# Performance work log

Hardware: AMD Instinct MI355X
Metric: run time of the kernel (lower is better)

## Reference

```python
import jax, jax.numpy as jnp
import numpy as np

ALPHA = 1.0
EPS = 1e-12  # tf.nn.l2_normalize epsilon


def setup_inputs() -> dict:
    key = jax.random.key(0)
    k1, k2 = jax.random.split(key)
    B, I, J, D, K = 32, 32, 32, 128, 64
    features = jax.random.normal(k1, (B, I, J, D), dtype=jnp.float32)
    kmeans_centers = jax.random.normal(k2, (B, K, D), dtype=jnp.float32)
    return {"features": features, "kmeans_centers": kmeans_centers}


def reference(features, kmeans_centers):
    # features: (B, I, J, D); kmeans_centers: (B, K, D)
    B = features.shape[0]
    # Squared distance ||f - c||^2 expanded to avoid materializing (B,I,J,K,D)
    f2 = jnp.sum(features * features, axis=-1)[..., None]          # (B,I,J,1)
    c2 = jnp.sum(kmeans_centers * kmeans_centers, axis=-1)[:, None, None, :]  # (B,1,1,K)
    fc = jnp.einsum('bijd,bkd->bijk', features, kmeans_centers)     # (B,I,J,K)
    d2 = f2 - 2.0 * fc + c2                                         # (B,I,J,K)
    sim = jax.nn.softmax(-ALPHA * d2, axis=-1)                      # (B,I,J,K)
    # vlad[b,k,d] = sum_ij sim[b,i,j,k] * (f[b,i,j,d] - c[b,k,d])
    vlad = (jnp.einsum('bijk,bijd->bkd', sim, features)
            - jnp.sum(sim, axis=(1, 2))[..., None] * kmeans_centers)  # (B,K,D)
    flat = vlad.reshape(B, -1)                                      # (B, K*D)
    # K.l2_normalize with axis=None -> normalize over ALL elements (global norm)
    norm = jnp.sqrt(jnp.maximum(jnp.sum(flat * flat), EPS))
    return flat / norm
```

## Files before the change

kernel.cpp:

```cpp
#include <hip/hip_runtime.h>


#define NB    32
#define SPLIT 16

typedef short short8 __attribute__((ext_vector_type(8)));
typedef float f32x4  __attribute__((ext_vector_type(4)));

__device__ __forceinline__ float bf2f(unsigned short u) {
    return __uint_as_float(((unsigned)u) << 16);
}
__device__ __forceinline__ unsigned short f2bf(float f) {
    unsigned u = __float_as_uint(f);
    return (unsigned short)((u + 0x7fffu + ((u >> 16) & 1u)) >> 16);
}
__device__ __forceinline__ int swz3(int x) { return (x ^ (x >> 3)) & 7; }

__global__ __launch_bounds__(256, 2)
void netvlad_main(const float* __restrict__ feat,
                  const float* __restrict__ cent,
                  float* __restrict__ partial,
                  float* __restrict__ ssumG)
{
    __shared__ __align__(16) char smem[58624];
    ushort4*        centHi = (ushort4*)smem;
    ushort4*        centLo = (ushort4*)(smem + 16384);
    unsigned short* FT     = (unsigned short*)(smem + 32768);
    unsigned short* ST     = (unsigned short*)(smem + 49152);
    float*          c2L    = (float*)(smem + 57344);
    float*          ssumW  = (float*)(smem + 57600);

    const int tid = threadIdx.x;
    const int bs  = blockIdx.x;
    const int b   = bs >> 4;
    const int n0  = (bs & 15) * 64;

    const float4* cent4 = (const float4*)cent + (size_t)b * 2048;
    const float4* feat4 = (const float4*)feat + ((size_t)b * 1024 + n0) * 32;

    #pragma unroll
    for (int it = 0; it < 8; ++it) {
        int g  = it * 256 + tid;
        int k  = g >> 5;
        int d4 = g & 31;
        float4 v = cent4[g];
        ushort4 h, l;
        h.x = f2bf(v.x); l.x = f2bf(v.x - bf2f(h.x));
        h.y = f2bf(v.y); l.y = f2bf(v.y - bf2f(h.y));
        h.z = f2bf(v.z); l.z = f2bf(v.z - bf2f(h.z));
        h.w = f2bf(v.w); l.w = f2bf(v.w - bf2f(h.w));
        int idx = k * 32 + (d4 ^ ((k & 7) << 1));
        centHi[idx] = h; centLo[idx] = l;
    }

    const int w    = tid >> 6;
    const int lane = tid & 63;
    const int lr   = lane & 15;
    const int lg   = lane >> 4;
    const int prow = 16 * w + lr;

    short8 ah[4], al[4];
    #pragma unroll
    for (int kt = 0; kt < 4; ++kt) {
        float4 fa = feat4[prow * 32 + kt * 8 + 2 * lg + 0];
        float4 fb = feat4[prow * 32 + kt * 8 + 2 * lg + 1];
        float fv[8] = { fa.x, fa.y, fa.z, fa.w, fb.x, fb.y, fb.z, fb.w };
        #pragma unroll
        for (int j = 0; j < 8; ++j) {
            unsigned short h = f2bf(fv[j]);
            ah[kt][j] = (short)h;
            al[kt][j] = (short)f2bf(fv[j] - bf2f(h));
            int d = kt * 32 + 8 * lg + j;
            FT[d * 64 + ((((prow >> 3) ^ swz3(d))) << 3) + (prow & 7)] = h;
        }
    }
    __syncthreads();

    if (tid < 64) {
        int k = tid;
        float a = 0.f;
        #pragma unroll
        for (int d4 = 0; d4 < 32; ++d4) {
            int idx = k * 32 + (d4 ^ ((k & 7) << 1));
            ushort4 h = centHi[idx], l = centLo[idx];
            float c0 = bf2f(h.x) + bf2f(l.x);
            float c1 = bf2f(h.y) + bf2f(l.y);
            float c2v = bf2f(h.z) + bf2f(l.z);
            float c3 = bf2f(h.w) + bf2f(l.w);
            a += c0 * c0 + c1 * c1 + c2v * c2v + c3 * c3;
        }
        c2L[k] = a;
    }
    __syncthreads();

    float c2r[4];
    #pragma unroll
    for (int nt = 0; nt < 4; ++nt) c2r[nt] = c2L[nt * 16 + lr];

    f32x4 acc[4];
    #pragma unroll
    for (int nt = 0; nt < 4; ++nt) acc[nt] = (f32x4){0.f, 0.f, 0.f, 0.f};
    #pragma unroll
    for (int kt = 0; kt < 4; ++kt) {
        #pragma unroll
        for (int nt = 0; nt < 4; ++nt) {
            int c  = nt * 16 + lr;
            int ch = c * 16 + ((kt * 4 + lg) ^ (c & 7));
            short8 bh = *(const short8*)(smem + ch * 16);
            short8 bl = *(const short8*)(smem + 16384 + ch * 16);
            acc[nt] = __builtin_amdgcn_mfma_f32_16x16x32_bf16(ah[kt], bh, acc[nt], 0, 0, 0);
            acc[nt] = __builtin_amdgcn_mfma_f32_16x16x32_bf16(ah[kt], bl, acc[nt], 0, 0, 0);
            acc[nt] = __builtin_amdgcn_mfma_f32_16x16x32_bf16(al[kt], bh, acc[nt], 0, 0, 0);
        }
    }

    float ssp[4] = {0.f, 0.f, 0.f, 0.f};
    #pragma unroll
    for (int r = 0; r < 4; ++r) {
        float s[4];
        #pragma unroll
        for (int nt = 0; nt < 4; ++nt) s[nt] = 2.f * acc[nt][r] - c2r[nt];
        float m = fmaxf(fmaxf(s[0], s[1]), fmaxf(s[2], s[3]));
        #pragma unroll
        for (int o = 8; o >= 1; o >>= 1) m = fmaxf(m, __shfl_xor(m, o));
        float e[4], t = 0.f;
        #pragma unroll
        for (int nt = 0; nt < 4; ++nt) { e[nt] = __expf(s[nt] - m); t += e[nt]; }
        #pragma unroll
        for (int o = 8; o >= 1; o >>= 1) t += __shfl_xor(t, o);
        float inv = __builtin_amdgcn_rcpf(t);
        int p = 16 * w + 4 * lg + r;
        #pragma unroll
        for (int nt = 0; nt < 4; ++nt) {
            int k = nt * 16 + lr;
            float val = e[nt] * inv;
            ssp[nt] += val;
            ST[k * 64 + ((((p >> 3) ^ swz3(k))) << 3) + (p & 7)] = f2bf(val);
        }
    }
    #pragma unroll
    for (int nt = 0; nt < 4; ++nt) {
        float v = ssp[nt];
        v += __shfl_xor(v, 16);
        v += __shfl_xor(v, 32);
        if (lg == 0) ssumW[w * 64 + nt * 16 + lr] = v;
    }
    __syncthreads();

    if (tid < 64)
        ssumG[bs * 64 + tid] = ssumW[tid] + ssumW[64 + tid] + ssumW[128 + tid] + ssumW[192 + tid];

    f32x4 vac[8];
    #pragma unroll
    for (int dt = 0; dt < 8; ++dt) vac[dt] = (f32x4){0.f, 0.f, 0.f, 0.f};
    const int krow = 16 * w + lr;
    #pragma unroll
    for (int ks = 0; ks < 2; ++ks) {
        int cA = (ks * 4 + lg) ^ swz3(krow);
        short8 af = *(const short8*)(ST + krow * 64 + (cA << 3));
        #pragma unroll
        for (int dt = 0; dt < 8; ++dt) {
            int d  = dt * 16 + lr;
            int cB = (ks * 4 + lg) ^ swz3(d);
            short8 bf = *(const short8*)(FT + d * 64 + (cB << 3));
            vac[dt] = __builtin_amdgcn_mfma_f32_16x16x32_bf16(af, bf, vac[dt], 0, 0, 0);
        }
    }

    float* outp = partial + (size_t)bs * 8192;
    #pragma unroll
    for (int r = 0; r < 4; ++r) {
        int k = 16 * w + 4 * lg + r;
        #pragma unroll
        for (int dt = 0; dt < 8; ++dt)
            outp[k * 128 + dt * 16 + lr] = vac[dt][r];
    }
}

__global__ __launch_bounds__(256)
void netvlad_reduce(const float* __restrict__ partial,
                    const float* __restrict__ cent,
                    const float* __restrict__ ssumG,
                    float* __restrict__ vlad,
                    float* __restrict__ sqpart) {
    __shared__ float wsum[4];
    int idx = blockIdx.x * 256 + threadIdx.x;
    int b   = idx >> 11;
    int rem = idx & 2047;
    int k   = rem >> 5;
    const float4* p4 = (const float4*)partial;
    float4 a = make_float4(0.f, 0.f, 0.f, 0.f);
    float  ss = 0.f;
    #pragma unroll
    for (int s = 0; s < SPLIT; ++s) {
        float4 v = p4[((size_t)(b * SPLIT + s)) * 2048 + rem];
        a.x += v.x; a.y += v.y; a.z += v.z; a.w += v.w;
        ss += ssumG[(b * SPLIT + s) * 64 + k];
    }
    float4 c4 = ((const float4*)cent)[b * 2048 + rem];
    a.x -= ss * c4.x; a.y -= ss * c4.y; a.z -= ss * c4.z; a.w -= ss * c4.w;
    ((float4*)vlad)[idx] = a;
    float sq = a.x * a.x + a.y * a.y + a.z * a.z + a.w * a.w;
    #pragma unroll
    for (int o = 32; o >= 1; o >>= 1) sq += __shfl_xor(sq, o);
    if ((threadIdx.x & 63) == 0) wsum[threadIdx.x >> 6] = sq;
    __syncthreads();
    if (threadIdx.x == 0) sqpart[blockIdx.x] = wsum[0] + wsum[1] + wsum[2] + wsum[3];
}

__global__ __launch_bounds__(256)
void netvlad_norm(const float* __restrict__ vlad,
                  const float* __restrict__ sqpart,
                  float* __restrict__ out) {
    const float4* sq4 = (const float4*)sqpart;
    float4 v = sq4[threadIdx.x & 63];
    float t = v.x + v.y + v.z + v.w;
    #pragma unroll
    for (int o = 32; o >= 1; o >>= 1) t += __shfl_xor(t, o);
    float inv = __builtin_amdgcn_rcpf(sqrtf(fmaxf(t, 1e-12f)));
    int idx = blockIdx.x * 256 + threadIdx.x;
    float4 x = ((const float4*)vlad)[idx];
    ((float4*)out)[idx] = make_float4(x.x * inv, x.y * inv, x.z * inv, x.w * inv);
}

extern "C" void kernel_launch(void* const* d_in, const int* in_sizes, int n_in,
                              void* d_out, int out_size, void* d_ws, size_t ws_size,
                              hipStream_t stream) {
    const float* feat = (const float*)d_in[0];
    const float* cent = (const float*)d_in[1];
    float* out = (float*)d_out;

    char* ws = (char*)d_ws;
    const size_t partial_bytes = (size_t)NB * SPLIT * 64 * 128 * sizeof(float);
    const size_t vlad_bytes    = (size_t)NB * 64 * 128 * sizeof(float);
    const size_t ssum_bytes    = (size_t)NB * SPLIT * 64 * sizeof(float);
    float* partial = (float*)ws;
    float* vlad    = (float*)(ws + partial_bytes);
    float* ssumG   = (float*)(ws + partial_bytes + vlad_bytes);
    float* sqpart  = (float*)(ws + partial_bytes + vlad_bytes + ssum_bytes);

    netvlad_main  <<<NB * SPLIT, 256, 0, stream>>>(feat, cent, partial, ssumG);
    netvlad_reduce<<<256, 256, 0, stream>>>(partial, cent, ssumG, vlad, sqpart);
    netvlad_norm  <<<256, 256, 0, stream>>>(vlad, sqpart, out);
}
```

Measured before the change: 79.23 us.

## Halve split count with 512-thread blocks and fuse reduce+norm via grid barrier

The main kernel now processes 128 feature rows per block with 8 waves, which halves the number of partial VLAD tiles written and re-read by the reduction. The c2 computation is spread across all threads and reads fp32 centers directly. The reduce and normalize kernels are merged into one, which uses an atomic sum and a spin-wait grid barrier so the vlad buffer no longer round-trips through memory and one launch is removed. The spin barrier assumes all 256 finish blocks are co-resident, and the halved grid gives less parallelism in the main kernel.

```diff
diff --git a/kernel.cpp b/kernel.cpp
--- a/kernel.cpp
+++ b/kernel.cpp
@@ -2,7 +2,7 @@
 
 
 #define NB    32
-#define SPLIT 16
+#define SPLIT 8
 
 typedef short short8 __attribute__((ext_vector_type(8)));
 typedef float f32x4  __attribute__((ext_vector_type(4)));
@@ -14,33 +14,58 @@
     unsigned u = __float_as_uint(f);
     return (unsigned short)((u + 0x7fffu + ((u >> 16) & 1u)) >> 16);
 }
-__device__ __forceinline__ int swz3(int x) { return (x ^ (x >> 3)) & 7; }
-
-__global__ __launch_bounds__(256, 2)
+
+__global__ __launch_bounds__(512, 1)
 void netvlad_main(const float* __restrict__ feat,
                   const float* __restrict__ cent,
                   float* __restrict__ partial,
-                  float* __restrict__ ssumG)
+                  float* __restrict__ ssumG,
+                  float* __restrict__ sqG,
+                  unsigned int* __restrict__ ctr)
 {
-    __shared__ __align__(16) char smem[58624];
+    __shared__ __align__(16) char smem[84224];
     ushort4*        centHi = (ushort4*)smem;
     ushort4*        centLo = (ushort4*)(smem + 16384);
     unsigned short* FT     = (unsigned short*)(smem + 32768);
-    unsigned short* ST     = (unsigned short*)(smem + 49152);
-    float*          c2L    = (float*)(smem + 57344);
-    float*          ssumW  = (float*)(smem + 57600);
+    unsigned short* ST     = (unsigned short*)(smem + 65536);
+    float*          c2L    = (float*)(smem + 81920);
+    float*          ssumW  = (float*)(smem + 82176);
 
     const int tid = threadIdx.x;
     const int bs  = blockIdx.x;
-    const int b   = bs >> 4;
-    const int n0  = (bs & 15) * 64;
+    const int b   = bs >> 3;
+    const int n0  = (bs & 7) * 128;
+
+    if (bs == 0 && tid == 0) { sqG[0] = 0.f; ctr[0] = 0u; }
 
     const float4* cent4 = (const float4*)cent + (size_t)b * 2048;
     const float4* feat4 = (const float4*)feat + ((size_t)b * 1024 + n0) * 32;
 
-    #pragma unroll
-    for (int it = 0; it < 8; ++it) {
-        int g  = it * 256 + tid;
+    const int w    = tid >> 6;
+    const int lane = tid & 63;
+    const int lr   = lane & 15;
+    const int lg   = lane >> 4;
+    const int prow = 16 * w + lr;
+
+    short8 ah[4], al[4];
+    #pragma unroll
+    for (int kt = 0; kt < 4; ++kt) {
+        float4 fa = feat4[prow * 32 + kt * 8 + 2 * lg + 0];
+        float4 fb = feat4[prow * 32 + kt * 8 + 2 * lg + 1];
+        float fv[8] = { fa.x, fa.y, fa.z, fa.w, fb.x, fb.y, fb.z, fb.w };
+        #pragma unroll
+        for (int j = 0; j < 8; ++j) {
+            unsigned short h = f2bf(fv[j]);
+            ah[kt][j] = (short)h;
+            al[kt][j] = (short)f2bf(fv[j] - bf2f(h));
+            int d = kt * 32 + 8 * lg + j;
+            FT[d * 128 + ((((prow >> 3) ^ (d & 15))) << 3) + (prow & 7)] = h;
+        }
+    }
+
+    #pragma unroll
+    for (int it = 0; it < 4; ++it) {
+        int g  = it * 512 + tid;
         int k  = g >> 5;
         int d4 = g & 31;
         float4 v = cent4[g];
@@ -53,43 +78,18 @@
         centHi[idx] = h; centLo[idx] = l;
     }
 
-    const int w    = tid >> 6;
-    const int lane = tid & 63;
-    const int lr   = lane & 15;
-    const int lg   = lane >> 4;
-    const int prow = 16 * w + lr;
-
-    short8 ah[4], al[4];
-    #pragma unroll
-    for (int kt = 0; kt < 4; ++kt) {
-        float4 fa = feat4[prow * 32 + kt * 8 + 2 * lg + 0];
-        float4 fb = feat4[prow * 32 + kt * 8 + 2 * lg + 1];
-        float fv[8] = { fa.x, fa.y, fa.z, fa.w, fb.x, fb.y, fb.z, fb.w };
-        #pragma unroll
-        for (int j = 0; j < 8; ++j) {
-            unsigned short h = f2bf(fv[j]);
-            ah[kt][j] = (short)h;
-            al[kt][j] = (short)f2bf(fv[j] - bf2f(h));
-            int d = kt * 32 + 8 * lg + j;
-            FT[d * 64 + ((((prow >> 3) ^ swz3(d))) << 3) + (prow & 7)] = h;
-        }
-    }
-    __syncthreads();
-
-    if (tid < 64) {
-        int k = tid;
+    {
+        int k = tid >> 3, q = tid & 7;
         float a = 0.f;
         #pragma unroll
-        for (int d4 = 0; d4 < 32; ++d4) {
-            int idx = k * 32 + (d4 ^ ((k & 7) << 1));
-            ushort4 h = centHi[idx], l = centLo[idx];
-            float c0 = bf2f(h.x) + bf2f(l.x);
-            float c1 = bf2f(h.y) + bf2f(l.y);
-            float c2v = bf2f(h.z) + bf2f(l.z);
-            float c3 = bf2f(h.w) + bf2f(l.w);
-            a += c0 * c0 + c1 * c1 + c2v * c2v + c3 * c3;
-        }
-        c2L[k] = a;
+        for (int j = 0; j < 4; ++j) {
+            float4 v = cent4[k * 32 + q * 4 + j];
+            a += v.x * v.x + v.y * v.y + v.z * v.z + v.w * v.w;
+        }
+        a += __shfl_xor(a, 1);
+        a += __shfl_xor(a, 2);
+        a += __shfl_xor(a, 4);
+        if (q == 0) c2L[k] = a;
     }
     __syncthreads();
 
@@ -135,7 +135,7 @@
             int k = nt * 16 + lr;
             float val = e[nt] * inv;
             ssp[nt] += val;
-            ST[k * 64 + ((((p >> 3) ^ swz3(k))) << 3) + (p & 7)] = f2bf(val);
+            ST[k * 128 + ((((p >> 3) ^ (k & 15))) << 3) + (p & 7)] = f2bf(val);
         }
     }
     #pragma unroll
@@ -147,22 +147,28 @@
     }
     __syncthreads();
 
-    if (tid < 64)
-        ssumG[bs * 64 + tid] = ssumW[tid] + ssumW[64 + tid] + ssumW[128 + tid] + ssumW[192 + tid];
-
-    f32x4 vac[8];
-    #pragma unroll
-    for (int dt = 0; dt < 8; ++dt) vac[dt] = (f32x4){0.f, 0.f, 0.f, 0.f};
-    const int krow = 16 * w + lr;
-    #pragma unroll
-    for (int ks = 0; ks < 2; ++ks) {
-        int cA = (ks * 4 + lg) ^ swz3(krow);
-        short8 af = *(const short8*)(ST + krow * 64 + (cA << 3));
-        #pragma unroll
-        for (int dt = 0; dt < 8; ++dt) {
-            int d  = dt * 16 + lr;
-            int cB = (ks * 4 + lg) ^ swz3(d);
-            short8 bf = *(const short8*)(FT + d * 64 + (cB << 3));
+    if (tid < 64) {
+        float s = 0.f;
+        #pragma unroll
+        for (int ww = 0; ww < 8; ++ww) s += ssumW[ww * 64 + tid];
+        ssumG[bs * 64 + tid] = s;
+    }
+
+    f32x4 vac[4];
+    #pragma unroll
+    for (int dt = 0; dt < 4; ++dt) vac[dt] = (f32x4){0.f, 0.f, 0.f, 0.f};
+    const int kt2  = w & 3;
+    const int dh   = w >> 2;
+    const int krow = 16 * kt2 + lr;
+    #pragma unroll
+    for (int ks = 0; ks < 4; ++ks) {
+        int cA = (ks * 4 + lg) ^ (krow & 15);
+        short8 af = *(const short8*)(ST + krow * 128 + (cA << 3));
+        #pragma unroll
+        for (int dt = 0; dt < 4; ++dt) {
+            int d  = dh * 64 + dt * 16 + lr;
+            int cB = (ks * 4 + lg) ^ (d & 15);
+            short8 bf = *(const short8*)(FT + d * 128 + (cB << 3));
             vac[dt] = __builtin_amdgcn_mfma_f32_16x16x32_bf16(af, bf, vac[dt], 0, 0, 0);
         }
     }
@@ -170,21 +176,23 @@
     float* outp = partial + (size_t)bs * 8192;
     #pragma unroll
     for (int r = 0; r < 4; ++r) {
-        int k = 16 * w + 4 * lg + r;
-        #pragma unroll
-        for (int dt = 0; dt < 8; ++dt)
-            outp[k * 128 + dt * 16 + lr] = vac[dt][r];
+        int k = 16 * kt2 + 4 * lg + r;
+        #pragma unroll
+        for (int dt = 0; dt < 4; ++dt)
+            outp[k * 128 + dh * 64 + dt * 16 + lr] = vac[dt][r];
     }
 }
 
 __global__ __launch_bounds__(256)
-void netvlad_reduce(const float* __restrict__ partial,
+void netvlad_finish(const float* __restrict__ partial,
                     const float* __restrict__ cent,
                     const float* __restrict__ ssumG,
-                    float* __restrict__ vlad,
-                    float* __restrict__ sqpart) {
+                    float* __restrict__ sqG,
+                    unsigned int* __restrict__ ctr,
+                    float* __restrict__ out) {
     __shared__ float wsum[4];
-    int idx = blockIdx.x * 256 + threadIdx.x;
+    const int tid = threadIdx.x;
+    int idx = blockIdx.x * 256 + tid;
     int b   = idx >> 11;
     int rem = idx & 2047;
     int k   = rem >> 5;
@@ -199,28 +207,24 @@
     }
     float4 c4 = ((const float4*)cent)[b * 2048 + rem];
     a.x -= ss * c4.x; a.y -= ss * c4.y; a.z -= ss * c4.z; a.w -= ss * c4.w;
-    ((float4*)vlad)[idx] = a;
+
     float sq = a.x * a.x + a.y * a.y + a.z * a.z + a.w * a.w;
     #pragma unroll
     for (int o = 32; o >= 1; o >>= 1) sq += __shfl_xor(sq, o);
-    if ((threadIdx.x & 63) == 0) wsum[threadIdx.x >> 6] = sq;
-    __syncthreads();
-    if (threadIdx.x == 0) sqpart[blockIdx.x] = wsum[0] + wsum[1] + wsum[2] + wsum[3];
-}
-
-__global__ __launch_bounds__(256)
-void netvlad_norm(const float* __restrict__ vlad,
-                  const float* __restrict__ sqpart,
-                  float* __restrict__ out) {
-    const float4* sq4 = (const float4*)sqpart;
-    float4 v = sq4[threadIdx.x & 63];
-    float t = v.x + v.y + v.z + v.w;
-    #pragma unroll
-    for (int o = 32; o >= 1; o >>= 1) t += __shfl_xor(t, o);
+    if ((tid & 63) == 0) wsum[tid >> 6] = sq;
+    __syncthreads();
+    if (tid == 0) {
+        atomicAdd(sqG, wsum[0] + wsum[1] + wsum[2] + wsum[3]);
+        __threadfence();
+        atomicAdd(ctr, 1u);
+        while (__hip_atomic_load(ctr, __ATOMIC_ACQUIRE, __HIP_MEMORY_SCOPE_AGENT) < 256u)
+            __builtin_amdgcn_s_sleep(8);
+    }
+    __syncthreads();
+
+    float t = __hip_atomic_load(sqG, __ATOMIC_RELAXED, __HIP_MEMORY_SCOPE_AGENT);
     float inv = __builtin_amdgcn_rcpf(sqrtf(fmaxf(t, 1e-12f)));
-    int idx = blockIdx.x * 256 + threadIdx.x;
-    float4 x = ((const float4*)vlad)[idx];
-    ((float4*)out)[idx] = make_float4(x.x * inv, x.y * inv, x.z * inv, x.w * inv);
+    ((float4*)out)[idx] = make_float4(a.x * inv, a.y * inv, a.z * inv, a.w * inv);
 }
 
 extern "C" void kernel_launch(void* const* d_in, const int* in_sizes, int n_in,
@@ -232,14 +236,12 @@
 
     char* ws = (char*)d_ws;
     const size_t partial_bytes = (size_t)NB * SPLIT * 64 * 128 * sizeof(float);
-    const size_t vlad_bytes    = (size_t)NB * 64 * 128 * sizeof(float);
     const size_t ssum_bytes    = (size_t)NB * SPLIT * 64 * sizeof(float);
-    float* partial = (float*)ws;
-    float* vlad    = (float*)(ws + partial_bytes);
-    float* ssumG   = (float*)(ws + partial_bytes + vlad_bytes);
-    float* sqpart  = (float*)(ws + partial_bytes + vlad_bytes + ssum_bytes);
-
-    netvlad_main  <<<NB * SPLIT, 256, 0, stream>>>(feat, cent, partial, ssumG);
-    netvlad_reduce<<<256, 256, 0, stream>>>(partial, cent, ssumG, vlad, sqpart);
-    netvlad_norm  <<<256, 256, 0, stream>>>(vlad, sqpart, out);
-}
+    float*        partial = (float*)ws;
+    float*        ssumG   = (float*)(ws + partial_bytes);
+    float*        sqG     = (float*)(ws + partial_bytes + ssum_bytes);
+    unsigned int* ctr     = (unsigned int*)(ws + partial_bytes + ssum_bytes + 256);
+
+    netvlad_main  <<<NB * SPLIT, 512, 0, stream>>>(feat, cent, partial, ssumG, sqG, ctr);
+    netvlad_finish<<<NB * SPLIT, 256, 0, stream>>>(partial, cent, ssumG, sqG, ctr, out);
+}
```

After: 88.90 us. 1.12x slower.

## Precompute bf16 hi/lo center split and center norms in a prep kernel

Applied to the files above, without the earlier changes.

Adds a small prep kernel that converts the cluster centers into swizzled bf16 hi/lo pairs once per batch and computes their squared norms from the fp32 values. The main kernel then copies the prepared layout straight into shared memory and reads the norms from global memory, dropping its per-block conversion, the norm loop and one barrier. Before, that work was repeated by all 16 split blocks of each batch. The cost is an extra kernel launch plus a workspace round trip. The bf16 rounding helper also switches to the library intrinsic.

```diff
diff --git a/kernel.cpp b/kernel.cpp
--- a/kernel.cpp
+++ b/kernel.cpp
@@ -1,4 +1,5 @@
 #include <hip/hip_runtime.h>
+#include <hip/hip_bf16.h>
 
 
 #define NB    32
@@ -11,53 +12,75 @@
     return __uint_as_float(((unsigned)u) << 16);
 }
 __device__ __forceinline__ unsigned short f2bf(float f) {
-    unsigned u = __float_as_uint(f);
-    return (unsigned short)((u + 0x7fffu + ((u >> 16) & 1u)) >> 16);
+    __hip_bfloat16 h = __float2bfloat16(f);
+    unsigned short u;
+    __builtin_memcpy(&u, &h, 2);
+    return u;
 }
 __device__ __forceinline__ int swz3(int x) { return (x ^ (x >> 3)) & 7; }
+
+__global__ __launch_bounds__(256)
+void netvlad_prep(const float* __restrict__ cent,
+                  ushort4* __restrict__ cws,
+                  float* __restrict__ c2G) {
+    const int tid = threadIdx.x;
+    const int bi  = blockIdx.x;
+    const int b   = bi >> 3;
+    const int kg  = bi & 7;
+    const int kk  = tid >> 5;
+    const int d4  = tid & 31;
+    const int k   = kg * 8 + kk;
+    float4 v = ((const float4*)cent)[(size_t)b * 2048 + k * 32 + d4];
+    ushort4 h, l;
+    h.x = f2bf(v.x); l.x = f2bf(v.x - bf2f(h.x));
+    h.y = f2bf(v.y); l.y = f2bf(v.y - bf2f(h.y));
+    h.z = f2bf(v.z); l.z = f2bf(v.z - bf2f(h.z));
+    h.w = f2bf(v.w); l.w = f2bf(v.w - bf2f(h.w));
+    int slot = k * 32 + (d4 ^ ((k & 7) << 1));
+    cws[(size_t)b * 4096 + slot]        = h;
+    cws[(size_t)b * 4096 + 2048 + slot] = l;
+    float a = v.x * v.x + v.y * v.y + v.z * v.z + v.w * v.w;
+    a += __shfl_xor(a, 1);
+    a += __shfl_xor(a, 2);
+    a += __shfl_xor(a, 4);
+    a += __shfl_xor(a, 8);
+    a += __shfl_xor(a, 16);
+    if (d4 == 0) c2G[b * 64 + k] = a;
+}
 
 __global__ __launch_bounds__(256, 2)
 void netvlad_main(const float* __restrict__ feat,
-                  const float* __restrict__ cent,
+                  const ushort4* __restrict__ cws,
+                  const float* __restrict__ c2G,
                   float* __restrict__ partial,
                   float* __restrict__ ssumG)
 {
-    __shared__ __align__(16) char smem[58624];
-    ushort4*        centHi = (ushort4*)smem;
-    ushort4*        centLo = (ushort4*)(smem + 16384);
-    unsigned short* FT     = (unsigned short*)(smem + 32768);
-    unsigned short* ST     = (unsigned short*)(smem + 49152);
-    float*          c2L    = (float*)(smem + 57344);
-    float*          ssumW  = (float*)(smem + 57600);
+    __shared__ __align__(16) char smem[58368];
+    unsigned short* FT    = (unsigned short*)(smem + 32768);
+    unsigned short* ST    = (unsigned short*)(smem + 49152);
+    float*          ssumW = (float*)(smem + 57344);
 
     const int tid = threadIdx.x;
     const int bs  = blockIdx.x;
     const int b   = bs >> 4;
     const int n0  = (bs & 15) * 64;
 
-    const float4* cent4 = (const float4*)cent + (size_t)b * 2048;
+    const uint4* csrc = (const uint4*)(cws + (size_t)b * 4096);
+    #pragma unroll
+    for (int it = 0; it < 8; ++it)
+        ((uint4*)smem)[it * 256 + tid] = csrc[it * 256 + tid];
+
     const float4* feat4 = (const float4*)feat + ((size_t)b * 1024 + n0) * 32;
-
-    #pragma unroll
-    for (int it = 0; it < 8; ++it) {
-        int g  = it * 256 + tid;
-        int k  = g >> 5;
-        int d4 = g & 31;
-        float4 v = cent4[g];
-        ushort4 h, l;
-        h.x = f2bf(v.x); l.x = f2bf(v.x - bf2f(h.x));
-        h.y = f2bf(v.y); l.y = f2bf(v.y - bf2f(h.y));
-        h.z = f2bf(v.z); l.z = f2bf(v.z - bf2f(h.z));
-        h.w = f2bf(v.w); l.w = f2bf(v.w - bf2f(h.w));
-        int idx = k * 32 + (d4 ^ ((k & 7) << 1));
-        centHi[idx] = h; centLo[idx] = l;
-    }
 
     const int w    = tid >> 6;
     const int lane = tid & 63;
     const int lr   = lane & 15;
     const int lg   = lane >> 4;
     const int prow = 16 * w + lr;
+
+    float c2r[4];
+    #pragma unroll
+    for (int nt = 0; nt < 4; ++nt) c2r[nt] = c2G[b * 64 + nt * 16 + lr];
 
     short8 ah[4], al[4];
     #pragma unroll
@@ -75,27 +98,6 @@
         }
     }
     __syncthreads();
-
-    if (tid < 64) {
-        int k = tid;
-        float a = 0.f;
-        #pragma unroll
-        for (int d4 = 0; d4 < 32; ++d4) {
-            int idx = k * 32 + (d4 ^ ((k & 7) << 1));
-            ushort4 h = centHi[idx], l = centLo[idx];
-            float c0 = bf2f(h.x) + bf2f(l.x);
-            float c1 = bf2f(h.y) + bf2f(l.y);
-            float c2v = bf2f(h.z) + bf2f(l.z);
-            float c3 = bf2f(h.w) + bf2f(l.w);
-            a += c0 * c0 + c1 * c1 + c2v * c2v + c3 * c3;
-        }
-        c2L[k] = a;
-    }
-    __syncthreads();
-
-    float c2r[4];
-    #pragma unroll
-    for (int nt = 0; nt < 4; ++nt) c2r[nt] = c2L[nt * 16 + lr];
 
     f32x4 acc[4];
     #pragma unroll
@@ -232,14 +234,20 @@
 
     char* ws = (char*)d_ws;
     const size_t partial_bytes = (size_t)NB * SPLIT * 64 * 128 * sizeof(float);
+    const size_t cws_bytes     = (size_t)NB * 4096 * sizeof(ushort4);
+    const size_t c2_bytes      = (size_t)NB * 64 * sizeof(float);
     const size_t vlad_bytes    = (size_t)NB * 64 * 128 * sizeof(float);
     const size_t ssum_bytes    = (size_t)NB * SPLIT * 64 * sizeof(float);
-    float* partial = (float*)ws;
-    float* vlad    = (float*)(ws + partial_bytes);
-    float* ssumG   = (float*)(ws + partial_bytes + vlad_bytes);
-    float* sqpart  = (float*)(ws + partial_bytes + vlad_bytes + ssum_bytes);
-
-    netvlad_main  <<<NB * SPLIT, 256, 0, stream>>>(feat, cent, partial, ssumG);
+
+    float*   partial = (float*)ws;
+    ushort4* cwsp    = (ushort4*)(ws + partial_bytes);
+    float*   c2G     = (float*)(ws + partial_bytes + cws_bytes);
+    float*   vlad    = (float*)(ws + partial_bytes + cws_bytes + c2_bytes);
+    float*   ssumG   = (float*)(ws + partial_bytes + cws_bytes + c2_bytes + vlad_bytes);
+    float*   sqpart  = (float*)(ws + partial_bytes + cws_bytes + c2_bytes + vlad_bytes + ssum_bytes);
+
+    netvlad_prep  <<<256, 256, 0, stream>>>(cent, cwsp, c2G);
+    netvlad_main  <<<NB * SPLIT, 256, 0, stream>>>(feat, cwsp, c2G, partial, ssumG);
     netvlad_reduce<<<256, 256, 0, stream>>>(partial, cent, ssumG, vlad, sqpart);
     netvlad_norm  <<<256, 256, 0, stream>>>(vlad, sqpart, out);
 }
```

After: 79.87 us. No clear change (+0.8%).
